# Kernel tuning notes

Hardware: AMD Instinct MI355X
Metric: run time of the kernel (lower is better)

Reference implementation:

```python
import jax, jax.numpy as jnp
import numpy as np

DECAY = 0.6
GAIN = 0.4


def _layernorm(x, g, b, eps=1e-5):
    m = x.mean(-1, keepdims=True)
    v = x.var(-1, keepdims=True)
    return (x - m) * jax.lax.rsqrt(v + eps) * g + b


def _ema_scan(x, axis, reverse=False):
    # linear recurrence state = 0.6*state + 0.4*x as an associative scan
    a = jnp.full_like(x, DECAY)
    b = GAIN * x
    def comb(c1, c2):
        a1, b1 = c1
        a2, b2 = c2
        return a1 * a2, a2 * b1 + b2
    _, y = jax.lax.associative_scan(comb, (a, b), axis=axis, reverse=reverse)
    return y


def setup_inputs() -> dict:
    key = jax.random.key(0)
    B, H, W, D = 16, 64, 64, 384
    inner = 2 * D
    hidden = 4 * D
    ks = jax.random.split(key, 12)
    s = 0.02
    return {
        "x": jax.random.normal(ks[0], (B, H, W, D), jnp.float32),
        "n1_g": jnp.ones((D,), jnp.float32),
        "n1_b": jnp.zeros((D,), jnp.float32),
        "w_in": s * jax.random.normal(ks[1], (D, inner), jnp.float32),
        "b_in": jnp.zeros((inner,), jnp.float32),
        "k_conv": s * jax.random.normal(ks[2], (3, 3, 1, inner), jnp.float32),  # depthwise HWIO
        "on_g": jnp.ones((inner,), jnp.float32),
        "on_b": jnp.zeros((inner,), jnp.float32),
        "w_out": s * jax.random.normal(ks[3], (inner, D), jnp.float32),
        "b_out": jnp.zeros((D,), jnp.float32),
        "n2_g": jnp.ones((D,), jnp.float32),
        "n2_b": jnp.zeros((D,), jnp.float32),
        "w1": s * jax.random.normal(ks[4], (D, hidden), jnp.float32),
        "b1": jnp.zeros((hidden,), jnp.float32),
        "w2": s * jax.random.normal(ks[5], (hidden, D), jnp.float32),
        "b2": jnp.zeros((D,), jnp.float32),
    }


def reference(x, n1_g, n1_b, w_in, b_in, k_conv, on_g, on_b, w_out, b_out,
              n2_g, n2_b, w1, b1, w2, b2):
    inner = w_in.shape[1]
    # --- LegacyScan2DOperator branch ---
    h = _layernorm(x, n1_g, n1_b)
    p = h @ w_in + b_in  # [B,H,W,inner]
    local = jax.lax.conv_general_dilated(
        p, k_conv, window_strides=(1, 1), padding="SAME",
        dimension_numbers=("NHWC", "HWIO", "NHWC"),
        feature_group_count=inner)
    lr = _ema_scan(local, axis=2)                 # left->right over W
    rl = _ema_scan(local, axis=2, reverse=True)   # right->left
    tb = _ema_scan(local, axis=1)                 # top->bottom over H
    bt = _ema_scan(local, axis=1, reverse=True)   # bottom->top
    mixed = 0.25 * (lr + rl + tb + bt) + local
    mixed = _layernorm(mixed, on_g, on_b)
    x = x + (mixed @ w_out + b_out)
    # --- MLP branch ---
    h2 = _layernorm(x, n2_g, n2_b)
    m = jax.nn.gelu(h2 @ w1 + b1, approximate=False) @ w2 + b2
    return x + m
```

## Files before the change

kernel.cpp:

```cpp
#include <hip/hip_runtime.h>
#include <math.h>


typedef __attribute__((ext_vector_type(8))) short bf16x8;
typedef __attribute__((ext_vector_type(4))) float f32x4;

#define T_TOKENS 65536
#define DMODEL 384
#define DINNER 768
#define DHIDDEN 1536

__device__ __forceinline__ float bf2f(unsigned short u) {
  unsigned int x = ((unsigned int)u) << 16;
  return __builtin_bit_cast(float, x);
}
__device__ __forceinline__ unsigned short f2bf(float f) {
  unsigned int x = __builtin_bit_cast(unsigned int, f);
  x += 0x7fffu + ((x >> 16) & 1u);
  return (unsigned short)(x >> 16);
}
__device__ __forceinline__ void unpack2(unsigned int u, float& lo, float& hi) {
  lo = __builtin_bit_cast(float, u << 16);
  hi = __builtin_bit_cast(float, u & 0xffff0000u);
}
__device__ __forceinline__ unsigned int pack2(float lo, float hi) {
  return (unsigned int)f2bf(lo) | ((unsigned int)f2bf(hi) << 16);
}
__device__ __forceinline__ unsigned int pack2t(float lo, float hi) {
  return (__builtin_bit_cast(unsigned int, lo) >> 16) |
         (__builtin_bit_cast(unsigned int, hi) & 0xffff0000u);
}

__device__ __forceinline__ void gload16(const void* g, void* l) {
  __builtin_amdgcn_global_load_lds(
      (const __attribute__((address_space(1))) void*)g,
      (__attribute__((address_space(3))) void*)l, 16, 0, 0);
}

__global__ __launch_bounds__(256) void ln_fused_f32_384(
    const float* __restrict__ in, const float* __restrict__ g,
    const float* __restrict__ b, unsigned short* __restrict__ out) {
  const int tok = blockIdx.x * 4 + (threadIdx.x >> 6);
  const int lane = threadIdx.x & 63;
  const float2* row = (const float2*)(in + (size_t)tok * 384);
  float2 v[3];
  float s = 0.f, ss = 0.f;
#pragma unroll
  for (int k = 0; k < 3; k++) {
    v[k] = row[lane + 64 * k];
    s += v[k].x + v[k].y;
    ss += v[k].x * v[k].x + v[k].y * v[k].y;
  }
#pragma unroll
  for (int off = 32; off > 0; off >>= 1) {
    s += __shfl_xor(s, off);
    ss += __shfl_xor(ss, off);
  }
  const float m = s * (1.0f / 384.0f);
  const float r = rsqrtf(ss * (1.0f / 384.0f) - m * m + 1e-5f);
  unsigned int* op = (unsigned int*)(out + (size_t)tok * 384);
#pragma unroll
  for (int k = 0; k < 3; k++) {
    const int c = lane + 64 * k;
    const float2 gg = ((const float2*)g)[c];
    const float2 bb = ((const float2*)b)[c];
    op[c] = pack2((v[k].x - m) * r * gg.x + bb.x, (v[k].y - m) * r * gg.y + bb.y);
  }
}

__global__ __launch_bounds__(256) void ln_bundle_768(
    const uint2* __restrict__ mixed, const float* __restrict__ g,
    const float* __restrict__ b, uint2* __restrict__ out) {
  const int tid = threadIdx.x;
  const int tk = tid >> 2, j = tid & 3;
  const int token = blockIdx.x * 64 + tk;
  const int bb_ = token >> 12, posb = token & 4095;
  const size_t slab = (size_t)bb_ * 4096 + posb;
  float s = 0.f, ss = 0.f;
#pragma unroll 1
  for (int cg = j; cg < 192; cg += 4) {
    const uint2 v = mixed[((size_t)cg * 16) * 4096 + slab];
    float e0, e1, e2, e3;
    unpack2(v.x, e0, e1);
    unpack2(v.y, e2, e3);
    s += (e0 + e1) + (e2 + e3);
    ss += e0 * e0 + e1 * e1 + e2 * e2 + e3 * e3;
  }
  s += __shfl_xor(s, 1); ss += __shfl_xor(ss, 1);
  s += __shfl_xor(s, 2); ss += __shfl_xor(ss, 2);
  const float m = s * (1.0f / 768.0f);
  const float r = rsqrtf(ss * (1.0f / 768.0f) - m * m + 1e-5f);
  const size_t tokbase = (size_t)token * 192;
#pragma unroll 1
  for (int cg = j; cg < 192; cg += 4) {
    const uint2 v = mixed[((size_t)cg * 16) * 4096 + slab];
    const float4 gg = ((const float4*)g)[cg];
    const float4 bb4 = ((const float4*)b)[cg];
    float e0, e1, e2, e3;
    unpack2(v.x, e0, e1);
    unpack2(v.y, e2, e3);
    uint2 o;
    o.x = pack2((e0 - m) * r * gg.x + bb4.x, (e1 - m) * r * gg.y + bb4.y);
    o.y = pack2((e2 - m) * r * gg.z + bb4.z, (e3 - m) * r * gg.w + bb4.w);
    out[tokbase + cg] = o;
  }
}

__global__ __launch_bounds__(256) void wprep_kernel(const float* __restrict__ in,
                                                    unsigned short* __restrict__ out,
                                                    int K, int N) {
  __shared__ float t[32][33];
  const int k0 = blockIdx.x * 32, n0 = blockIdx.y * 32;
  const int a = threadIdx.x & 31, b8 = threadIdx.x >> 5;
#pragma unroll
  for (int i = 0; i < 4; i++)
    t[b8 + 8 * i][a] = in[(size_t)(k0 + b8 + 8 * i) * N + n0 + a];
  __syncthreads();
#pragma unroll
  for (int i = 0; i < 4; i++)
    out[(size_t)(n0 + b8 + 8 * i) * K + k0 + a] = f2bf(t[a][b8 + 8 * i]);
}

template <int EPI>
__global__ __launch_bounds__(256, 4) void gemm_bt_kernel(
    const unsigned short* __restrict__ A, int lda,
    const unsigned short* __restrict__ Bt, int ldb, int KT,
    const float* __restrict__ bias, const float* __restrict__ res,
    void* __restrict__ C, int ldc, int nby) {
  __shared__ unsigned short smem[16640];
  char* const smc = (char*)smem;

  const int tid = threadIdx.x;
  const int w = tid >> 6, lane = tid & 63;
  const int cpx = gridDim.x >> 3;
  const int g = blockIdx.x;
  const int sw = (g & 7) * cpx + (g >> 3);
  const int bx = sw / nby, by = sw - bx * nby;
  const int tok0 = bx << 7, n0 = by << 7;

  const int wm = w >> 1, wn = w & 1;
  const int lrow = lane & 15, kgrp = lane >> 4;

  const int lr4 = lane >> 2;
  const int r0 = (w * 2 + 0) * 16 + lr4;
  const int r1 = (w * 2 + 1) * 16 + lr4;
  const int c0 = ((lane & 3) ^ ((r0 >> 1) & 3)) << 3;
  const int c1 = ((lane & 3) ^ ((r1 >> 1) & 3)) << 3;
  const unsigned short* A0 = A + (size_t)(tok0 + r0) * lda + c0;
  const unsigned short* A1p = A + (size_t)(tok0 + r1) * lda + c1;
  const unsigned short* B0 = Bt + (size_t)(n0 + r0) * ldb + c0;
  const unsigned short* B1 = Bt + (size_t)(n0 + r1) * ldb + c1;
  const int d0 = (w * 2 + 0) * 1024;
  const int d1 = (w * 2 + 1) * 1024;

  f32x4 acc[4][4];
#pragma unroll
  for (int i = 0; i < 4; i++)
#pragma unroll
    for (int j = 0; j < 4; j++) {
      f32x4 z = {0.f, 0.f, 0.f, 0.f};
      acc[i][j] = z;
    }

  const int nt = KT >> 5;
  gload16(A0, smc + d0);
  gload16(A1p, smc + d1);
  gload16(B0, smc + 16384 + d0);
  gload16(B1, smc + 16384 + d1);
  __syncthreads();

  int buf = 0;
  for (int t = 0; t < nt; t++) {
    if (t + 1 < nt) {
      const int kt = (t + 1) << 5;
      const int bo = (buf ^ 1) * 8192;
      gload16(A0 + kt, smc + bo + d0);
      gload16(A1p + kt, smc + bo + d1);
      gload16(B0 + kt, smc + 16384 + bo + d0);
      gload16(B1 + kt, smc + 16384 + bo + d1);
    }
    const int bo = buf * 8192;
    bf16x8 af[4], bf_[4];
#pragma unroll
    for (int f = 0; f < 4; f++) {
      const int ra = wm * 64 + f * 16 + lrow;
      const int rb = wn * 64 + f * 16 + lrow;
      af[f] = *(const bf16x8*)(smc + bo + ra * 64 +
                               ((kgrp ^ ((ra >> 1) & 3)) << 4));
      bf_[f] = *(const bf16x8*)(smc + 16384 + bo + rb * 64 +
                                ((kgrp ^ ((rb >> 1) & 3)) << 4));
    }
#pragma unroll
    for (int mf = 0; mf < 4; mf++)
#pragma unroll
      for (int nf = 0; nf < 4; nf++)
        acc[mf][nf] = __builtin_amdgcn_mfma_f32_16x16x32_bf16(
            af[mf], bf_[nf], acc[mf][nf], 0, 0, 0);
    __syncthreads();
    buf ^= 1;
  }

  if constexpr (EPI == 3) {
#pragma unroll
    for (int mf = 0; mf < 4; mf++)
#pragma unroll
      for (int nf = 0; nf < 4; nf++) {
        const int cl = wn * 64 + nf * 16 + lrow;
        const float bv = bias[n0 + cl];
#pragma unroll
        for (int r = 0; r < 4; r++) {
          const int tl = wm * 64 + mf * 16 + kgrp * 4 + r;
          smem[(cl >> 2) * 520 + tl * 4 + (cl & 3)] =
              f2bf(acc[mf][nf][r] + bv);
        }
      }
    __syncthreads();
    const int bb_ = tok0 >> 12, pos0 = tok0 & 4095, cg0 = n0 >> 2;
    uint2* Cb = (uint2*)C;
#pragma unroll
    for (int e = 0; e < 16; e++) {
      const int lin = e * 256 + tid;
      const int cgl = lin >> 7, pp = lin & 127;
      const uint2 v = *(const uint2*)&smem[cgl * 520 + pp * 4];
      Cb[((size_t)(cg0 + cgl) * 16 + bb_) * 4096 + pos0 + pp] = v;
    }
  } else {
#pragma unroll
    for (int mf = 0; mf < 4; mf++) {
#pragma unroll
      for (int nf = 0; nf < 4; nf++) {
        const int gcol = n0 + wn * 64 + nf * 16 + lrow;
        const float bv = bias ? bias[gcol] : 0.0f;
#pragma unroll
        for (int r = 0; r < 4; r++) {
          const int grow = tok0 + wm * 64 + mf * 16 + kgrp * 4 + r;
          float v = acc[mf][nf][r] + bv;
          const size_t idx = (size_t)grow * ldc + gcol;
          if constexpr (EPI == 1) {
            ((float*)C)[idx] = v + res[idx];
          } else {
            const float z = 1.5957691216057308f * (v + 0.044715f * v * v * v);
            const float gl = v / (1.0f + __expf(-z));
            ((unsigned short*)C)[idx] = f2bf(gl);
          }
        }
      }
    }
  }
}

__device__ __forceinline__ void ema_seg_f(const unsigned int vals[16],
                                          const int seg, float rl[16],
                                          float rh[16]) {
  const float A16 = 2.8211099e-4f;
  const float A32 = 7.9586611e-8f;
  float a, bv, t;
  float za = 0.f, zb = 0.f;
#pragma unroll
  for (int j = 0; j < 16; j++) {
    unpack2(vals[j], a, bv);
    za = 0.6f * za + 0.4f * a;
    zb = 0.6f * zb + 0.4f * bv;
  }
  t = __shfl_up(za, 1); if (seg >= 1) za += A16 * t;
  t = __shfl_up(zb, 1); if (seg >= 1) zb += A16 * t;
  t = __shfl_up(za, 2); if (seg >= 2) za += A32 * t;
  t = __shfl_up(zb, 2); if (seg >= 2) zb += A32 * t;
  float yfa = __shfl_up(za, 1), yfb = __shfl_up(zb, 1);
  if (seg == 0) { yfa = 0.f; yfb = 0.f; }
  float ua = 0.f, ub = 0.f;
#pragma unroll
  for (int j = 15; j >= 0; j--) {
    unpack2(vals[j], a, bv);
    ua = 0.6f * ua + 0.4f * a;
    ub = 0.6f * ub + 0.4f * bv;
  }
  t = __shfl_down(ua, 1); if (seg <= 2) ua += A16 * t;
  t = __shfl_down(ub, 1); if (seg <= 2) ub += A16 * t;
  t = __shfl_down(ua, 2); if (seg <= 1) ua += A32 * t;
  t = __shfl_down(ub, 2); if (seg <= 1) ub += A32 * t;
  float zba = __shfl_down(ua, 1), zbb = __shfl_down(ub, 1);
  if (seg == 3) { zba = 0.f; zbb = 0.f; }
  float fa = yfa, fb = yfb;
#pragma unroll
  for (int j = 0; j < 16; j++) {
    unpack2(vals[j], a, bv);
    fa = 0.6f * fa + 0.4f * a;
    fb = 0.6f * fb + 0.4f * bv;
    rl[j] = fa;
    rh[j] = fb;
  }
  float ga = zba, gb = zbb;
#pragma unroll
  for (int j = 15; j >= 0; j--) {
    unpack2(vals[j], a, bv);
    ga = 0.6f * ga + 0.4f * a;
    gb = 0.6f * gb + 0.4f * bv;
    rl[j] = 0.25f * (rl[j] + ga);
    rh[j] = 0.25f * (rh[j] + gb);
  }
}

__global__ __launch_bounds__(512) void conv_scan_kernel(
    const uint2* __restrict__ p, const float* __restrict__ kconv,
    uint2* __restrict__ mixed) {
  __shared__ unsigned int loc[2][64][65];
  __shared__ float klds[36];
  const int tid = threadIdx.x;
  const int c = blockIdx.x;
  const int b = blockIdx.y;
  const uint2* pb = p + ((size_t)c * 16 + b) * 4096;

  if (tid < 36) klds[tid] = kconv[(tid >> 2) * DINNER + c * 4 + (tid & 3)];
  __syncthreads();

#pragma unroll 1
  for (int i = 0; i < 8; i++) {
    const int pos = tid + 512 * i;
    const int h = pos >> 6, w = pos & 63;
    float a0 = 0.f, a1 = 0.f, a2 = 0.f, a3 = 0.f;
#pragma unroll
    for (int dh = 0; dh < 3; dh++) {
      const int hh = h + dh - 1;
      const bool vh = (unsigned)hh < 64u;
      const int hcl = min(max(hh, 0), 63);
#pragma unroll
      for (int dw = 0; dw < 3; dw++) {
        const int ww = w + dw - 1;
        const bool vv = vh && ((unsigned)ww < 64u);
        const int wcl = min(max(ww, 0), 63);
        uint2 pv = pb[hcl * 64 + wcl];
        if (!vv) { pv.x = 0; pv.y = 0; }
        const int t = dh * 3 + dw;
        float lo, hi;
        unpack2(pv.x, lo, hi);
        a0 += lo * klds[t * 4 + 0];
        a1 += hi * klds[t * 4 + 1];
        unpack2(pv.y, lo, hi);
        a2 += lo * klds[t * 4 + 2];
        a3 += hi * klds[t * 4 + 3];
      }
    }
    loc[0][h][w] = pack2t(a0, a1);
    loc[1][h][w] = pack2t(a2, a3);
  }
  __syncthreads();

  const int seg = tid & 3;
  const int ax = (tid >> 2) & 63;
  const int cp = tid >> 8;
  const int j0 = seg * 16;

  float hcl_[16], hch_[16];
  {
    unsigned int vals[16];
#pragma unroll
    for (int j = 0; j < 16; j++) vals[j] = loc[cp][j0 + j][ax];
    ema_seg_f(vals, seg, hcl_, hch_);
  }
  __syncthreads();

  {
    unsigned int vals[16];
    float wl[16], wh[16];
#pragma unroll
    for (int j = 0; j < 16; j++) vals[j] = loc[cp][ax][j0 + j];
    ema_seg_f(vals, seg, wl, wh);
#pragma unroll
    for (int j = 0; j < 16; j++) {
      float a, bv;
      unpack2(vals[j], a, bv);
      loc[cp][ax][j0 + j] = pack2t(a + wl[j], bv + wh[j]);
    }
  }
  __syncthreads();

#pragma unroll
  for (int j = 0; j < 16; j++) {
    float a, bv;
    unpack2(loc[cp][j0 + j][ax], a, bv);
    loc[cp][j0 + j][ax] = pack2t(a + hcl_[j], bv + hch_[j]);
  }
  __syncthreads();

  uint2* mb = mixed + ((size_t)c * 16 + b) * 4096;
#pragma unroll 1
  for (int i = 0; i < 8; i++) {
    const int pos = tid + 512 * i;
    const int h = pos >> 6, w = pos & 63;
    uint2 st;
    st.x = loc[0][h][w];
    st.y = loc[1][h][w];
    mb[pos] = st;
  }
}

extern "C" void kernel_launch(void* const* d_in, const int* in_sizes, int n_in,
                              void* d_out, int out_size, void* d_ws,
                              size_t ws_size, hipStream_t stream) {
  const float* x = (const float*)d_in[0];
  const float* n1_g = (const float*)d_in[1];
  const float* n1_b = (const float*)d_in[2];
  const float* w_in = (const float*)d_in[3];
  const float* b_in = (const float*)d_in[4];
  const float* k_conv = (const float*)d_in[5];
  const float* on_g = (const float*)d_in[6];
  const float* on_b = (const float*)d_in[7];
  const float* w_out = (const float*)d_in[8];
  const float* b_out = (const float*)d_in[9];
  const float* n2_g = (const float*)d_in[10];
  const float* n2_b = (const float*)d_in[11];
  const float* w1 = (const float*)d_in[12];
  const float* b1 = (const float*)d_in[13];
  const float* w2 = (const float*)d_in[14];
  const float* b2 = (const float*)d_in[15];

  const size_t MB = 1024 * 1024;
  char* ws = (char*)d_ws;
  unsigned short* R1 = (unsigned short*)(ws + 3 * MB / 2);
  unsigned short* R2 = (unsigned short*)(ws + 3 * MB / 2 + 96 * MB);

  unsigned short* A1 = R2;
  unsigned short* wTin = R2 + (48 * MB) / 2;
  unsigned short* p = R1;
  unsigned short* A2 = R2;
  unsigned short* wTout = R1;
  unsigned short* A3 = R1;
  unsigned short* wT1 = R1 + (48 * MB) / 2;
  unsigned short* wT2 = wT1 + (size_t)1536 * 384;
  unsigned short* gb = R2;

  float* out = (float*)d_out;
  dim3 b256(256);

  ln_fused_f32_384<<<T_TOKENS / 4, b256, 0, stream>>>(x, n1_g, n1_b, A1);
  wprep_kernel<<<dim3(12, 24), b256, 0, stream>>>(w_in, wTin, DMODEL, DINNER);
  gemm_bt_kernel<3><<<3072, b256, 0, stream>>>(A1, DMODEL, wTin, DMODEL, DMODEL,
                                               b_in, nullptr, p, DINNER, 6);
  conv_scan_kernel<<<dim3(192, 16), dim3(512), 0, stream>>>(
      (const uint2*)p, k_conv, (uint2*)p);
  ln_bundle_768<<<1024, b256, 0, stream>>>((const uint2*)p, on_g, on_b,
                                           (uint2*)A2);
  wprep_kernel<<<dim3(24, 12), b256, 0, stream>>>(w_out, wTout, DINNER, DMODEL);
  gemm_bt_kernel<1><<<1536, b256, 0, stream>>>(A2, DINNER, wTout, DINNER, DINNER,
                                               b_out, x, out, DMODEL, 3);
  ln_fused_f32_384<<<T_TOKENS / 4, b256, 0, stream>>>(out, n2_g, n2_b, A3);
  wprep_kernel<<<dim3(12, 48), b256, 0, stream>>>(w1, wT1, DMODEL, DHIDDEN);
  wprep_kernel<<<dim3(48, 12), b256, 0, stream>>>(w2, wT2, DHIDDEN, DMODEL);
  for (int hh = 0; hh < 2; hh++) {
    const size_t toff = (size_t)hh * 32768;
    gemm_bt_kernel<2><<<3072, b256, 0, stream>>>(
        A3 + toff * DMODEL, DMODEL, wT1, DMODEL, DMODEL, b1, nullptr, gb,
        DHIDDEN, 12);
    gemm_bt_kernel<1><<<768, b256, 0, stream>>>(
        gb, DHIDDEN, wT2, DHIDDEN, DHIDDEN, b2, out + toff * DMODEL,
        out + toff * DMODEL, DMODEL, 3);
  }
}
```

Before: 663.6 us.

## Fuse depthwise conv into register-held W-scan and merge weight-prep launches

The depthwise 3x3 conv is now computed per thread directly into registers along its 16-element W segment. The left-right EMA scan then runs on those registers instead of first writing the conv result to LDS and reading it back, which removes one LDS round trip and one barrier phase. The three later weight transpose/convert kernels are merged into a single launch to cut launch overhead. In exchange, the conv reads 4-byte values per channel pair from global memory in a less coalesced pattern, and each thread does more loads and carries more registers.

```diff
diff --git a/kernel.cpp b/kernel.cpp
--- a/kernel.cpp
+++ b/kernel.cpp
@@ -106,19 +106,45 @@
   }
 }
 
+__device__ __forceinline__ void wprep_tile(const float* __restrict__ in,
+                                           unsigned short* __restrict__ out,
+                                           int K, int N, int k0, int n0,
+                                           int tid, float t[32][33]) {
+  const int a = tid & 31, b8 = tid >> 5;
+#pragma unroll
+  for (int i = 0; i < 4; i++)
+    t[b8 + 8 * i][a] = in[(size_t)(k0 + b8 + 8 * i) * N + n0 + a];
+  __syncthreads();
+#pragma unroll
+  for (int i = 0; i < 4; i++)
+    out[(size_t)(n0 + b8 + 8 * i) * K + k0 + a] = f2bf(t[a][b8 + 8 * i]);
+}
+
 __global__ __launch_bounds__(256) void wprep_kernel(const float* __restrict__ in,
                                                     unsigned short* __restrict__ out,
                                                     int K, int N) {
   __shared__ float t[32][33];
-  const int k0 = blockIdx.x * 32, n0 = blockIdx.y * 32;
-  const int a = threadIdx.x & 31, b8 = threadIdx.x >> 5;
-#pragma unroll
-  for (int i = 0; i < 4; i++)
-    t[b8 + 8 * i][a] = in[(size_t)(k0 + b8 + 8 * i) * N + n0 + a];
-  __syncthreads();
-#pragma unroll
-  for (int i = 0; i < 4; i++)
-    out[(size_t)(n0 + b8 + 8 * i) * K + k0 + a] = f2bf(t[a][b8 + 8 * i]);
+  wprep_tile(in, out, K, N, blockIdx.x * 32, blockIdx.y * 32, threadIdx.x, t);
+}
+
+__global__ __launch_bounds__(256) void wprep3_kernel(
+    const float* __restrict__ wout, unsigned short* __restrict__ wToutp,
+    const float* __restrict__ w1, unsigned short* __restrict__ wT1p,
+    const float* __restrict__ w2, unsigned short* __restrict__ wT2p) {
+  __shared__ float t[32][33];
+  int id = blockIdx.x;
+  if (id < 288) {
+    wprep_tile(wout, wToutp, 768, 384, (id / 12) * 32, (id % 12) * 32,
+               threadIdx.x, t);
+  } else if (id < 864) {
+    id -= 288;
+    wprep_tile(w1, wT1p, 384, 1536, (id / 48) * 32, (id % 48) * 32,
+               threadIdx.x, t);
+  } else {
+    id -= 864;
+    wprep_tile(w2, wT2p, 1536, 384, (id / 12) * 32, (id % 12) * 32,
+               threadIdx.x, t);
+  }
 }
 
 template <int EPI>
@@ -301,6 +327,54 @@
   }
 }
 
+__device__ __forceinline__ void ema_seg_ff(const float vlo[16],
+                                           const float vhi[16], const int seg,
+                                           float rl[16], float rh[16]) {
+  const float A16 = 2.8211099e-4f;
+  const float A32 = 7.9586611e-8f;
+  float t;
+  float za = 0.f, zb = 0.f;
+#pragma unroll
+  for (int j = 0; j < 16; j++) {
+    za = 0.6f * za + 0.4f * vlo[j];
+    zb = 0.6f * zb + 0.4f * vhi[j];
+  }
+  t = __shfl_up(za, 1); if (seg >= 1) za += A16 * t;
+  t = __shfl_up(zb, 1); if (seg >= 1) zb += A16 * t;
+  t = __shfl_up(za, 2); if (seg >= 2) za += A32 * t;
+  t = __shfl_up(zb, 2); if (seg >= 2) zb += A32 * t;
+  float yfa = __shfl_up(za, 1), yfb = __shfl_up(zb, 1);
+  if (seg == 0) { yfa = 0.f; yfb = 0.f; }
+  float ua = 0.f, ub = 0.f;
+#pragma unroll
+  for (int j = 15; j >= 0; j--) {
+    ua = 0.6f * ua + 0.4f * vlo[j];
+    ub = 0.6f * ub + 0.4f * vhi[j];
+  }
+  t = __shfl_down(ua, 1); if (seg <= 2) ua += A16 * t;
+  t = __shfl_down(ub, 1); if (seg <= 2) ub += A16 * t;
+  t = __shfl_down(ua, 2); if (seg <= 1) ua += A32 * t;
+  t = __shfl_down(ub, 2); if (seg <= 1) ub += A32 * t;
+  float zba = __shfl_down(ua, 1), zbb = __shfl_down(ub, 1);
+  if (seg == 3) { zba = 0.f; zbb = 0.f; }
+  float fa = yfa, fb = yfb;
+#pragma unroll
+  for (int j = 0; j < 16; j++) {
+    fa = 0.6f * fa + 0.4f * vlo[j];
+    fb = 0.6f * fb + 0.4f * vhi[j];
+    rl[j] = fa;
+    rh[j] = fb;
+  }
+  float ga = zba, gb = zbb;
+#pragma unroll
+  for (int j = 15; j >= 0; j--) {
+    ga = 0.6f * ga + 0.4f * vlo[j];
+    gb = 0.6f * gb + 0.4f * vhi[j];
+    rl[j] = 0.25f * (rl[j] + ga);
+    rh[j] = 0.25f * (rh[j] + gb);
+  }
+}
+
 __global__ __launch_bounds__(512) void conv_scan_kernel(
     const uint2* __restrict__ p, const float* __restrict__ kconv,
     uint2* __restrict__ mixed) {
@@ -309,41 +383,9 @@
   const int tid = threadIdx.x;
   const int c = blockIdx.x;
   const int b = blockIdx.y;
-  const uint2* pb = p + ((size_t)c * 16 + b) * 4096;
+  const unsigned int* pbu = (const unsigned int*)(p + ((size_t)c * 16 + b) * 4096);
 
   if (tid < 36) klds[tid] = kconv[(tid >> 2) * DINNER + c * 4 + (tid & 3)];
-  __syncthreads();
-
-#pragma unroll 1
-  for (int i = 0; i < 8; i++) {
-    const int pos = tid + 512 * i;
-    const int h = pos >> 6, w = pos & 63;
-    float a0 = 0.f, a1 = 0.f, a2 = 0.f, a3 = 0.f;
-#pragma unroll
-    for (int dh = 0; dh < 3; dh++) {
-      const int hh = h + dh - 1;
-      const bool vh = (unsigned)hh < 64u;
-      const int hcl = min(max(hh, 0), 63);
-#pragma unroll
-      for (int dw = 0; dw < 3; dw++) {
-        const int ww = w + dw - 1;
-        const bool vv = vh && ((unsigned)ww < 64u);
-        const int wcl = min(max(ww, 0), 63);
-        uint2 pv = pb[hcl * 64 + wcl];
-        if (!vv) { pv.x = 0; pv.y = 0; }
-        const int t = dh * 3 + dw;
-        float lo, hi;
-        unpack2(pv.x, lo, hi);
-        a0 += lo * klds[t * 4 + 0];
-        a1 += hi * klds[t * 4 + 1];
-        unpack2(pv.y, lo, hi);
-        a2 += lo * klds[t * 4 + 2];
-        a3 += hi * klds[t * 4 + 3];
-      }
-    }
-    loc[0][h][w] = pack2t(a0, a1);
-    loc[1][h][w] = pack2t(a2, a3);
-  }
   __syncthreads();
 
   const int seg = tid & 3;
@@ -351,6 +393,60 @@
   const int cp = tid >> 8;
   const int j0 = seg * 16;
 
+  float alo[16], ahi[16];
+  {
+    float klo[9], khi[9];
+#pragma unroll
+    for (int t = 0; t < 9; t++) {
+      klo[t] = klds[t * 4 + cp * 2 + 0];
+      khi[t] = klds[t * 4 + cp * 2 + 1];
+    }
+#pragma unroll
+    for (int j = 0; j < 16; j++) { alo[j] = 0.f; ahi[j] = 0.f; }
+    const bool vtop = ax > 0, vbot = ax < 63;
+    const int rt = (ax > 0 ? ax - 1 : 0) * 64;
+    const int rm = ax * 64;
+    const int rb_ = (ax < 63 ? ax + 1 : 63) * 64;
+#pragma unroll
+    for (int cc = -1; cc <= 16; cc++) {
+      const int col = j0 + cc;
+      const bool vc = (unsigned)col < 64u;
+      const int ccl = vc ? col : 0;
+      float tlo = 0.f, thi = 0.f, mlo = 0.f, mhi = 0.f, blo = 0.f, bhi = 0.f;
+      if (vc) {
+        unsigned int um = pbu[(rm + ccl) * 2 + cp];
+        unpack2(um, mlo, mhi);
+        if (vtop) {
+          unsigned int ut = pbu[(rt + ccl) * 2 + cp];
+          unpack2(ut, tlo, thi);
+        }
+        if (vbot) {
+          unsigned int ub = pbu[(rb_ + ccl) * 2 + cp];
+          unpack2(ub, blo, bhi);
+        }
+      }
+#pragma unroll
+      for (int dw = 0; dw < 3; dw++) {
+        const int o = cc + 1 - dw;
+        if (o >= 0 && o < 16) {
+          alo[o] += tlo * klo[dw] + mlo * klo[3 + dw] + blo * klo[6 + dw];
+          ahi[o] += thi * khi[dw] + mhi * khi[3 + dw] + bhi * khi[6 + dw];
+        }
+      }
+    }
+  }
+  unsigned int wvals[16];
+  {
+#pragma unroll
+    for (int j = 0; j < 16; j++) loc[cp][ax][j0 + j] = pack2t(alo[j], ahi[j]);
+    float wl[16], wh[16];
+    ema_seg_ff(alo, ahi, seg, wl, wh);
+#pragma unroll
+    for (int j = 0; j < 16; j++)
+      wvals[j] = pack2t(alo[j] + wl[j], ahi[j] + wh[j]);
+  }
+  __syncthreads();
+
   float hcl_[16], hch_[16];
   {
     unsigned int vals[16];
@@ -360,19 +456,8 @@
   }
   __syncthreads();
 
-  {
-    unsigned int vals[16];
-    float wl[16], wh[16];
-#pragma unroll
-    for (int j = 0; j < 16; j++) vals[j] = loc[cp][ax][j0 + j];
-    ema_seg_f(vals, seg, wl, wh);
-#pragma unroll
-    for (int j = 0; j < 16; j++) {
-      float a, bv;
-      unpack2(vals[j], a, bv);
-      loc[cp][ax][j0 + j] = pack2t(a + wl[j], bv + wh[j]);
-    }
-  }
+#pragma unroll
+  for (int j = 0; j < 16; j++) loc[cp][ax][j0 + j] = wvals[j];
   __syncthreads();
 
 #pragma unroll
@@ -383,7 +468,7 @@
   }
   __syncthreads();
 
-  uint2* mb = mixed + ((size_t)c * 16 + b) * 4096;
+  uint2* mb = (uint2*)mixed + ((size_t)c * 16 + b) * 4096;
 #pragma unroll 1
   for (int i = 0; i < 8; i++) {
     const int pos = tid + 512 * i;
@@ -441,12 +526,10 @@
       (const uint2*)p, k_conv, (uint2*)p);
   ln_bundle_768<<<1024, b256, 0, stream>>>((const uint2*)p, on_g, on_b,
                                            (uint2*)A2);
-  wprep_kernel<<<dim3(24, 12), b256, 0, stream>>>(w_out, wTout, DINNER, DMODEL);
+  wprep3_kernel<<<1440, b256, 0, stream>>>(w_out, wTout, w1, wT1, w2, wT2);
   gemm_bt_kernel<1><<<1536, b256, 0, stream>>>(A2, DINNER, wTout, DINNER, DINNER,
                                                b_out, x, out, DMODEL, 3);
   ln_fused_f32_384<<<T_TOKENS / 4, b256, 0, stream>>>(out, n2_g, n2_b, A3);
-  wprep_kernel<<<dim3(12, 48), b256, 0, stream>>>(w1, wT1, DMODEL, DHIDDEN);
-  wprep_kernel<<<dim3(48, 12), b256, 0, stream>>>(w2, wT2, DHIDDEN, DMODEL);
   for (int hh = 0; hh < 2; hh++) {
     const size_t toff = (size_t)hh * 32768;
     gemm_bt_kernel<2><<<3072, b256, 0, stream>>>(
```

Result: slower. 741.7 us (+11.8%).
